# Optimization experiments

Hardware: AMD Instinct MI355X
Metric: run time of the kernel (lower is better)

## Reference

```python
import jax, jax.numpy as jnp
import numpy as np

D_MODEL = 256
N_LAYERS = 4
D_STATE = 16
EXPAND = 2
D_CONV = 4
D_INNER = EXPAND * D_MODEL
DT_RANK = (D_MODEL + 15) // 16  # ceil(d_model/16) = 16
BATCH = 8
SEQ = 2048
EPS = 1e-5


def setup_inputs() -> dict:
    key = jax.random.key(0)
    ks = jax.random.split(key, 12)
    rn = lambda k, s, sc=0.02: jax.random.normal(k, s, dtype=jnp.float32) * sc
    A_log = jnp.log(jnp.broadcast_to(jnp.arange(1, D_STATE + 1, dtype=jnp.float32),
                                     (N_LAYERS, D_INNER, D_STATE)))
    return {
        "x": jax.random.normal(ks[0], (BATCH, SEQ, 2), dtype=jnp.float32),
        "w_in": rn(ks[1], (D_MODEL, 2), 0.5),
        "b_in": jnp.zeros((D_MODEL,), jnp.float32),
        "norm_w": jnp.ones((N_LAYERS, D_MODEL), jnp.float32),
        "in_proj_w": rn(ks[2], (N_LAYERS, 2 * D_INNER, D_MODEL)),
        "conv_w": rn(ks[3], (N_LAYERS, D_INNER, 1, D_CONV), 0.1),
        "conv_b": jnp.zeros((N_LAYERS, D_INNER), jnp.float32),
        "x_proj_w": rn(ks[4], (N_LAYERS, DT_RANK + 2 * D_STATE, D_INNER)),
        "dt_proj_w": rn(ks[5], (N_LAYERS, D_INNER, DT_RANK), 0.1),
        "dt_proj_b": rn(ks[6], (N_LAYERS, D_INNER), 0.1),
        "A_log": A_log,
        "D_skip": jnp.ones((N_LAYERS, D_INNER), jnp.float32),
        "out_proj_w": rn(ks[7], (N_LAYERS, D_MODEL, D_INNER)),
        "w_head": rn(ks[8], (1, D_MODEL), 0.1),
        "b_head": jnp.zeros((1,), jnp.float32),
    }


def _rmsnorm(x, w):
    return x * jax.lax.rsqrt(jnp.mean(x * x, axis=-1, keepdims=True) + EPS) * w


def _causal_dw_conv(x, w, b):
    # x: (B, L, C); w: (C, 1, K) depthwise; causal left-pad K-1
    xt = jnp.swapaxes(x, 1, 2)  # (B, C, L)
    y = jax.lax.conv_general_dilated(xt, w, (1,), [(D_CONV - 1, 0)],
                                     dimension_numbers=("NCH", "OIH", "NCH"),
                                     feature_group_count=D_INNER)
    return jnp.swapaxes(y + b[None, :, None], 1, 2)


def _selective_scan(u, delta, A, Bm, Cm, Dp):
    # u, delta: (B, L, E); A: (E, N); Bm, Cm: (B, L, N); Dp: (E,)
    dA = jnp.exp(delta[..., None] * A)                 # (B, L, E, N)
    dBu = (delta * u)[..., None] * Bm[:, :, None, :]   # (B, L, E, N)

    def step(h, t):
        dA_t, dBu_t = t
        h = dA_t * h + dBu_t
        return h, h

    h0 = jnp.zeros((u.shape[0], A.shape[0], A.shape[1]), u.dtype)
    _, hs = jax.lax.scan(step, h0, (jnp.swapaxes(dA, 0, 1), jnp.swapaxes(dBu, 0, 1)))
    y = jnp.einsum("lben,bln->ble", hs, Cm)            # (B, L, E)
    return y + u * Dp


def _mamba_block(x, in_w, cw, cb, xp_w, dtw, dtb, A_log, Dp, out_w):
    xz = x @ in_w.T                                    # (B, L, 2E)
    u, z = jnp.split(xz, 2, axis=-1)
    u = jax.nn.silu(_causal_dw_conv(u, cw, cb))
    dbc = u @ xp_w.T                                   # (B, L, dt_rank + 2N)
    delta = jax.nn.softplus(dbc[..., :DT_RANK] @ dtw.T + dtb)
    Bm = dbc[..., DT_RANK:DT_RANK + D_STATE]
    Cm = dbc[..., DT_RANK + D_STATE:]
    y = _selective_scan(u, delta, -jnp.exp(A_log), Bm, Cm, Dp)
    return (y * jax.nn.silu(z)) @ out_w.T


def reference(x, w_in, b_in, norm_w, in_proj_w, conv_w, conv_b, x_proj_w,
              dt_proj_w, dt_proj_b, A_log, D_skip, out_proj_w, w_head, b_head):
    h = x @ w_in.T + b_in                              # (B, L, d_model)
    for i in range(N_LAYERS):
        h = h + _mamba_block(_rmsnorm(h, norm_w[i]), in_proj_w[i], conv_w[i],
                             conv_b[i], x_proj_w[i], dt_proj_w[i], dt_proj_b[i],
                             A_log[i], D_skip[i], out_proj_w[i])
    return (h @ w_head.T + b_head)[..., 0]             # (B, L)
```

## Files before the change

kernel.cpp:

```cpp
#include <hip/hip_runtime.h>
#include <hip/hip_bf16.h>

#define BATCH 8
#define SEQ   2048
#define DM    256
#define DI    512
#define DS    16
#define DTR   16
#define NL    4
#define ROWS  (BATCH*SEQ)
#define NCH   32
#define CHL   64
#define NF    576

typedef __attribute__((ext_vector_type(8))) __bf16 bh8;
typedef __attribute__((ext_vector_type(4))) float f4;

#if __has_builtin(__builtin_amdgcn_exp2f)
#define EXP2(x) __builtin_amdgcn_exp2f(x)
#else
#define EXP2(x) exp2f(x)
#endif
#define LOG2E 1.4426950408889634f

__device__ __forceinline__ float bf2f(unsigned short u) {
    union { unsigned int i; float f; } v; v.i = ((unsigned int)u) << 16; return v.f;
}
__device__ __forceinline__ float4 us4f(ushort4 q) {
    return make_float4(bf2f(q.x), bf2f(q.y), bf2f(q.z), bf2f(q.w));
}
__device__ __forceinline__ float ldg1(const void* p, int i, int bf) {
    if (bf) return bf2f(((const unsigned short*)p)[i]);
    return ((const float*)p)[i];
}
__device__ __forceinline__ float4 ldg4(const void* p, int i, int bf) {
    if (bf) return us4f(*(const ushort4*)(((const unsigned short*)p) + i));
    return *(const float4*)(((const float*)p) + i);
}
__device__ __forceinline__ unsigned short f2bs(float f) {
    union { float f; unsigned u; } x; x.f = f;
    unsigned r = (x.u + 0x7fffu + ((x.u >> 16) & 1u)) >> 16;
    return (unsigned short)r;
}
__device__ __forceinline__ float fsilu(float x) {
    return x * __builtin_amdgcn_rcpf(1.0f + __expf(-x));
}
__device__ __forceinline__ float fsoftplus(float x) {
    return (x > 15.0f) ? x : __logf(1.0f + __expf(x));
}
__device__ __forceinline__ void pow16(float e1, float* pw) {
    float p2 = e1 * e1, p3 = p2 * e1, p4 = p2 * p2;
    float p5 = p4 * e1, p6 = p4 * p2, p7 = p4 * p3, p8 = p4 * p4;
    pw[0] = e1; pw[1] = p2; pw[2] = p3; pw[3] = p4;
    pw[4] = p5; pw[5] = p6; pw[6] = p7; pw[7] = p8;
    pw[8]  = p8 * e1; pw[9]  = p8 * p2; pw[10] = p8 * p3; pw[11] = p8 * p4;
    pw[12] = p8 * p5; pw[13] = p8 * p6; pw[14] = p8 * p7; pw[15] = p8 * p8;
}

typedef const __attribute__((address_space(1))) unsigned int* gas_t;
typedef __attribute__((address_space(3))) unsigned int* las_t;
__device__ __forceinline__ void gl16(const void* g, void* l) {
    __builtin_amdgcn_global_load_lds((gas_t)g, (las_t)l, 16, 0, 0);
}

__global__ void k_probe(const void* x, const void* A_log, int* flag) {
    int t = threadIdx.x;
    float v = bf2f(((const unsigned short*)x)[2 * t]);
    int bad = (fabsf(v) < 32.0f) ? 0 : 1;
    for (int o = 1; o < 64; o <<= 1) bad += __shfl_xor(bad, o);
    int bf = (bad > 8) ? 0 : 1;
    int nb = 0;
    for (int j = 0; j < 64; j++) {
        int e = ((j * 64 + t) * 17) & 32767;
        int n = e & 15;
        float a = ldg1(A_log, e, bf);
        float ea = __expf(a);
        if (fabsf(ea - (float)(n + 1)) > 0.02f * (float)(n + 1)) nb = 1;
    }
    for (int o = 1; o < 64; o <<= 1) nb += __shfl_xor(nb, o);
    if (t == 0) { flag[0] = bf; flag[1] = (nb == 0) ? 1 : 0; }
}

__global__ __launch_bounds__(256) void k_prep(const void* dtw, const void* xpw,
                                              unsigned short* Wc, const int* flag) {
    int bf = *flag;
    int blk = blockIdx.x;
    int l = blk / NF, r = blk % NF;
    int t = threadIdx.x;
    unsigned short* out = Wc + ((size_t)l * NF + r) * DI;
#pragma unroll
    for (int p = 0; p < 2; p++) {
        int k = t + p * 256;
        float v = 0.0f;
        if (r < 512) {
            const int db = l * DI * DTR + r * DTR;
            const int xb = l * 48 * DI;
#pragma unroll
            for (int j = 0; j < 16; j++)
                v = fmaf(ldg1(dtw, db + j, bf), ldg1(xpw, xb + j * DI + k, bf), v);
        } else if (r < 544) {
            v = ldg1(xpw, l * 48 * DI + (16 + r - 512) * DI + k, bf);
        }
        out[k] = f2bs(v);
    }
}

__global__ __launch_bounds__(256) void k_inproj(const void* x, const void* w_in,
                                                const void* b_in, unsigned short* h, const int* flag) {
    int bf = *flag;
    int row = blockIdx.x, e = threadIdx.x;
    float x0 = ldg1(x, row * 2 + 0, bf), x1 = ldg1(x, row * 2 + 1, bf);
    float w0 = ldg1(w_in, e * 2 + 0, bf), w1 = ldg1(w_in, e * 2 + 1, bf);
    float bb = ldg1(b_in, e, bf);
    h[(size_t)row * DM + e] = f2bs(fmaf(x0, w0, fmaf(x1, w1, bb)));
}

__global__ __launch_bounds__(256) void k_rmsnorm(const unsigned short* h, const void* norm_w,
                                                 int w_off, unsigned short* xn, const int* flag) {
    int bf = *flag;
    int wv = threadIdx.x >> 6, ln = threadIdx.x & 63;
    int row = blockIdx.x * 4 + wv;
    float4 v = us4f(*(const ushort4*)(h + (size_t)row * DM + ln * 4));
    float ss = v.x * v.x + v.y * v.y + v.z * v.z + v.w * v.w;
    for (int o = 1; o < 64; o <<= 1) ss += __shfl_xor(ss, o);
    float sc = rsqrtf(ss / DM + 1e-5f);
    float4 w = ldg4(norm_w, w_off + ln * 4, bf);
    ushort4 o4 = { f2bs(v.x * sc * w.x), f2bs(v.y * sc * w.y),
                   f2bs(v.z * sc * w.z), f2bs(v.w * sc * w.w) };
    *(ushort4*)(xn + (size_t)row * DM + ln * 4) = o4;
}

#define ASTR 72

template <int BN, bool ADD>
__global__ __launch_bounds__(256, 4) void k_mfma(const unsigned short* A, const void* W, int w_off,
                                                 unsigned short* Cp, int N, int K, const int* flag) {
    int bf = *flag;
    __shared__ unsigned short SMEM[(128 + BN) * ASTR];
    unsigned short* As = SMEM;
    unsigned short* Ws = SMEM + 128 * 64;
    constexpr int NT = BN / 32;
    constexpr int TSTR = BN + 8;

    int bm = blockIdx.x, bn = blockIdx.y;
    int t = threadIdx.x;
    int w = t >> 6, lane = t & 63;
    int wm = w >> 1, wn = w & 1;
    int lr = lane & 15, quad = lane >> 4;
    int crow = lane >> 3;
    int ccol = ((lane & 7) ^ (lane >> 3)) * 8;

    f4 acc[4][NT];
#pragma unroll
    for (int i = 0; i < 4; i++)
#pragma unroll
        for (int j = 0; j < NT; j++) acc[i][j] = f4{0.f, 0.f, 0.f, 0.f};

    for (int k0 = 0; k0 < K; k0 += 64) {
        __syncthreads();
#pragma unroll
        for (int i = 0; i < 4; i++) {
            int ci = w * 4 + i;
            int r = ci * 8 + crow;
            gl16(A + (size_t)(bm * 128 + r) * K + k0 + ccol, &As[ci * 512]);
        }
        if (bf) {
#pragma unroll
            for (int i = 0; i < BN / 32; i++) {
                int ci = w * (BN / 32) + i;
                int r = ci * 8 + crow;
                gl16((const unsigned short*)W + (size_t)w_off +
                         (size_t)(bn * BN + r) * K + k0 + ccol,
                     &Ws[ci * 512]);
            }
        } else {
#pragma unroll
            for (int i = 0; i < BN * 8 / 256; i++) {
                int ch = t + i * 256;
                int r = ch >> 3, kc = (ch & 7) * 8;
                size_t off = (size_t)w_off + (size_t)(bn * BN + r) * K + k0 + kc;
                const float* src = (const float*)W + off;
                float4 a0 = *(const float4*)src;
                float4 a1 = *(const float4*)(src + 4);
                ushort4 v0 = { f2bs(a0.x), f2bs(a0.y), f2bs(a0.z), f2bs(a0.w) };
                ushort4 v1 = { f2bs(a1.x), f2bs(a1.y), f2bs(a1.z), f2bs(a1.w) };
                unsigned short* dst = &Ws[r * 64 + (kc ^ ((r & 7) << 3))];
                *(ushort4*)dst = v0;
                *(ushort4*)(dst + 4) = v1;
            }
        }
        __syncthreads();
#pragma unroll
        for (int ks = 0; ks < 64; ks += 32) {
            int csw = (ks + quad * 8) ^ ((lr & 7) << 3);
            bh8 af[4];
#pragma unroll
            for (int i = 0; i < 4; i++)
                af[i] = *(const bh8*)&As[(wm * 64 + i * 16 + lr) * 64 + csw];
            bh8 wf[NT];
#pragma unroll
            for (int j = 0; j < NT; j++)
                wf[j] = *(const bh8*)&Ws[(wn * (BN / 2) + j * 16 + lr) * 64 + csw];
#pragma unroll
            for (int i = 0; i < 4; i++)
#pragma unroll
                for (int j = 0; j < NT; j++)
                    acc[i][j] = __builtin_amdgcn_mfma_f32_16x16x32_bf16(af[i], wf[j], acc[i][j], 0, 0, 0);
        }
    }
    __syncthreads();
    unsigned short* Tile = SMEM;
#pragma unroll
    for (int i = 0; i < 4; i++) {
        int rl = wm * 64 + i * 16 + quad * 4;
#pragma unroll
        for (int j = 0; j < NT; j++) {
            int cl = wn * (BN / 2) + j * 16 + lr;
#pragma unroll
            for (int r = 0; r < 4; r++)
                Tile[(rl + r) * TSTR + cl] = f2bs(acc[i][j][r]);
        }
    }
    __syncthreads();
    constexpr int CPT = 128 * BN / 8 / 256;
#pragma unroll
    for (int i = 0; i < CPT; i++) {
        int ch = t + i * 256;
        int r = ch / (BN / 8), qc = (ch % (BN / 8)) * 8;
        uint4 v = *(uint4*)&Tile[r * TSTR + qc];
        size_t gidx = (size_t)(bm * 128 + r) * N + bn * BN + qc;
        if (ADD) {
            uint4 c = *(uint4*)&Cp[gidx];
            unsigned short* vp = (unsigned short*)&v;
            unsigned short* cp2 = (unsigned short*)&c;
            uint4 o;
            unsigned short* op = (unsigned short*)&o;
#pragma unroll
            for (int e = 0; e < 8; e++) op[e] = f2bs(bf2f(vp[e]) + bf2f(cp2[e]));
            *(uint4*)&Cp[gidx] = o;
        } else {
            *(uint4*)&Cp[gidx] = v;
        }
    }
}

__global__ __launch_bounds__(256, 4) void k_fused(const unsigned short* A, const unsigned short* Wc,
                                                  int w_off, unsigned short* delta, float* BC,
                                                  const void* dtb, int layer, const int* flag) {
    int bf = *flag;
    __shared__ unsigned short SMEM[(128 + 64) * ASTR];
    unsigned short* As = SMEM;
    unsigned short* Ws = SMEM + 128 * 64;
    constexpr int TSTR = 72;

    int bm = blockIdx.x, bn = blockIdx.y;
    int t = threadIdx.x;
    int w = t >> 6, lane = t & 63;
    int wm = w >> 1, wn = w & 1;
    int lr = lane & 15, quad = lane >> 4;
    int crow = lane >> 3;
    int ccol = ((lane & 7) ^ (lane >> 3)) * 8;

    f4 acc[4][2];
#pragma unroll
    for (int i = 0; i < 4; i++)
#pragma unroll
        for (int j = 0; j < 2; j++) acc[i][j] = f4{0.f, 0.f, 0.f, 0.f};

    for (int k0 = 0; k0 < DI; k0 += 64) {
        __syncthreads();
#pragma unroll
        for (int i = 0; i < 4; i++) {
            int ci = w * 4 + i;
            int r = ci * 8 + crow;
            gl16(A + (size_t)(bm * 128 + r) * DI + k0 + ccol, &As[ci * 512]);
        }
#pragma unroll
        for (int i = 0; i < 2; i++) {
            int ci = w * 2 + i;
            int r = ci * 8 + crow;
            gl16(Wc + (size_t)w_off + (size_t)(bn * 64 + r) * DI + k0 + ccol, &Ws[ci * 512]);
        }
        __syncthreads();
#pragma unroll
        for (int ks = 0; ks < 64; ks += 32) {
            int csw = (ks + quad * 8) ^ ((lr & 7) << 3);
            bh8 af[4];
#pragma unroll
            for (int i = 0; i < 4; i++)
                af[i] = *(const bh8*)&As[(wm * 64 + i * 16 + lr) * 64 + csw];
            bh8 wf[2];
#pragma unroll
            for (int j = 0; j < 2; j++)
                wf[j] = *(const bh8*)&Ws[(wn * 32 + j * 16 + lr) * 64 + csw];
#pragma unroll
            for (int i = 0; i < 4; i++)
#pragma unroll
                for (int j = 0; j < 2; j++)
                    acc[i][j] = __builtin_amdgcn_mfma_f32_16x16x32_bf16(af[i], wf[j], acc[i][j], 0, 0, 0);
        }
    }
    if (bn < 8) {
        __syncthreads();
        unsigned short* Tile = SMEM;
#pragma unroll
        for (int i = 0; i < 4; i++) {
            int rl = wm * 64 + i * 16 + quad * 4;
#pragma unroll
            for (int j = 0; j < 2; j++) {
                int cl = wn * 32 + j * 16 + lr;
                float bb = ldg1(dtb, layer * DI + bn * 64 + cl, bf);
#pragma unroll
                for (int r = 0; r < 4; r++)
                    Tile[(rl + r) * TSTR + cl] = f2bs(fsoftplus(acc[i][j][r] + bb));
            }
        }
        __syncthreads();
#pragma unroll
        for (int i = 0; i < 4; i++) {
            int ch = t + i * 256;
            int r = ch >> 3, qc = (ch & 7) * 8;
            uint4 v = *(uint4*)&Tile[r * TSTR + qc];
            *(uint4*)&delta[(size_t)(bm * 128 + r) * DI + bn * 64 + qc] = v;
        }
    } else {
#pragma unroll
        for (int i = 0; i < 4; i++) {
            int row0 = bm * 128 + wm * 64 + i * 16 + quad * 4;
#pragma unroll
            for (int j = 0; j < 2; j++) {
                int col = bn * 64 + wn * 32 + j * 16 + lr;
                if (col < 544) {
#pragma unroll
                    for (int r = 0; r < 4; r++)
                        BC[(size_t)(row0 + r) * 32 + (col - 512)] = acc[i][j][r];
                }
            }
        }
    }
}

__global__ __launch_bounds__(256) void k_conv(const unsigned short* xz, const void* cw, const void* cb,
                                              int layer, unsigned short* u, const int* flag) {
    int bf = *flag;
    int idx = blockIdx.x * 256 + threadIdx.x;
    int dq = idx & 127;
    int row = idx >> 7;
    int l = row & (SEQ - 1);
    int d = dq * 4;
    float4 w0 = ldg4(cw, (layer * DI + d + 0) * 4, bf);
    float4 w1 = ldg4(cw, (layer * DI + d + 1) * 4, bf);
    float4 w2 = ldg4(cw, (layer * DI + d + 2) * 4, bf);
    float4 w3 = ldg4(cw, (layer * DI + d + 3) * 4, bf);
    float4 bb = ldg4(cb, layer * DI + d, bf);
    const unsigned short* base = xz + (size_t)row * (2 * DI) + d;
    float4 t0 = make_float4(0, 0, 0, 0), t1 = t0, t2 = t0;
    if (l >= 3) t0 = us4f(*(const ushort4*)(base - 3 * 2 * DI));
    if (l >= 2) t1 = us4f(*(const ushort4*)(base - 2 * 2 * DI));
    if (l >= 1) t2 = us4f(*(const ushort4*)(base - 1 * 2 * DI));
    float4 t3 = us4f(*(const ushort4*)base);
    float a0 = bb.x; a0 = fmaf(w0.x, t0.x, a0); a0 = fmaf(w0.y, t1.x, a0); a0 = fmaf(w0.z, t2.x, a0); a0 = fmaf(w0.w, t3.x, a0);
    float a1 = bb.y; a1 = fmaf(w1.x, t0.y, a1); a1 = fmaf(w1.y, t1.y, a1); a1 = fmaf(w1.z, t2.y, a1); a1 = fmaf(w1.w, t3.y, a1);
    float a2 = bb.z; a2 = fmaf(w2.x, t0.z, a2); a2 = fmaf(w2.y, t1.z, a2); a2 = fmaf(w2.z, t2.z, a2); a2 = fmaf(w2.w, t3.z, a2);
    float a3 = bb.w; a3 = fmaf(w3.x, t0.w, a3); a3 = fmaf(w3.y, t1.w, a3); a3 = fmaf(w3.z, t2.w, a3); a3 = fmaf(w3.w, t3.w, a3);
    ushort4 o = { f2bs(fsilu(a0)), f2bs(fsilu(a1)), f2bs(fsilu(a2)), f2bs(fsilu(a3)) };
    *(ushort4*)(u + (size_t)row * DI + d) = o;
}

__global__ __launch_bounds__(256) void k_scan1(const unsigned short* delta, const unsigned short* u,
                                               const float* BC, const void* A_log, float* Sb, float* E,
                                               int layer, const int* flag) {
    int bf = flag[0], sA = flag[1];
    int x = blockIdx.x;
    int dg = x & 1, c = (x >> 1) & (NCH - 1), b = x >> 6;
    int tid = threadIdx.x;
    int d = dg * 256 + tid;
    int t0 = c * CHL;

    __shared__ float sB[CHL][16];
    {
        int r = tid >> 2, q = tid & 3;
        *(float4*)&sB[r][q * 4] =
            *(const float4*)(BC + ((size_t)b * SEQ + t0 + r) * 32 + q * 4);
    }

    float A2[16];
#pragma unroll
    for (int n4 = 0; n4 < 4; n4++) {
        float4 a4 = ldg4(A_log, (layer * DI + d) * DS + n4 * 4, bf);
        A2[n4 * 4 + 0] = -__expf(a4.x) * LOG2E;
        A2[n4 * 4 + 1] = -__expf(a4.y) * LOG2E;
        A2[n4 * 4 + 2] = -__expf(a4.z) * LOG2E;
        A2[n4 * 4 + 3] = -__expf(a4.w) * LOG2E;
    }
    float h[16];
#pragma unroll
    for (int n = 0; n < 16; n++) h[n] = 0.0f;
    float S = 0.0f;

    const unsigned short* dp = delta + ((size_t)b * SEQ + t0) * DI + d;
    const unsigned short* up = u + ((size_t)b * SEQ + t0) * DI + d;

    float dl0[4], uu0[4];
#pragma unroll
    for (int j = 0; j < 4; j++) { dl0[j] = bf2f(dp[j * DI]); uu0[j] = bf2f(up[j * DI]); }
    __syncthreads();

    for (int s = 0; s < CHL / 4; s++) {
        int sn = (s + 1 < CHL / 4) ? (s + 1) : s;
        float dl1[4], uu1[4];
#pragma unroll
        for (int j = 0; j < 4; j++) {
            dl1[j] = bf2f(dp[(sn * 4 + j) * DI]);
            uu1[j] = bf2f(up[(sn * 4 + j) * DI]);
        }
#pragma unroll
        for (int j = 0; j < 4; j++) {
            int t = s * 4 + j;
            float dlt = dl0[j], uu = uu0[j];
            float du = dlt * uu;
            S += dlt;
            if (sA) {
                float pw[16];
                pow16(EXP2(-dlt * LOG2E), pw);
#pragma unroll
                for (int n4 = 0; n4 < 4; n4++) {
                    float4 Bv = *(const float4*)&sB[t][n4 * 4];
                    int n = n4 * 4;
                    h[n + 0] = fmaf(pw[n + 0], h[n + 0], du * Bv.x);
                    h[n + 1] = fmaf(pw[n + 1], h[n + 1], du * Bv.y);
                    h[n + 2] = fmaf(pw[n + 2], h[n + 2], du * Bv.z);
                    h[n + 3] = fmaf(pw[n + 3], h[n + 3], du * Bv.w);
                }
            } else {
#pragma unroll
                for (int n4 = 0; n4 < 4; n4++) {
                    float4 Bv = *(const float4*)&sB[t][n4 * 4];
                    int n = n4 * 4;
                    float a0 = EXP2(dlt * A2[n + 0]); h[n + 0] = fmaf(a0, h[n + 0], du * Bv.x);
                    float a1 = EXP2(dlt * A2[n + 1]); h[n + 1] = fmaf(a1, h[n + 1], du * Bv.y);
                    float a2 = EXP2(dlt * A2[n + 2]); h[n + 2] = fmaf(a2, h[n + 2], du * Bv.z);
                    float a3 = EXP2(dlt * A2[n + 3]); h[n + 3] = fmaf(a3, h[n + 3], du * Bv.w);
                }
            }
        }
#pragma unroll
        for (int j = 0; j < 4; j++) { dl0[j] = dl1[j]; uu0[j] = uu1[j]; }
    }
    Sb[((size_t)b * NCH + c) * DI + d] = S;
    float* Ed = E + (((size_t)b * NCH + c) * DI + d) * DS;
#pragma unroll
    for (int n4 = 0; n4 < 4; n4++)
        *(float4*)(Ed + n4 * 4) = make_float4(h[n4 * 4], h[n4 * 4 + 1], h[n4 * 4 + 2], h[n4 * 4 + 3]);
}

__global__ __launch_bounds__(256) void k_stitch(const float* Sb, const void* A_log, float* E,
                                                int layer, const int* flag) {
    int bf = flag[0];
    int g = blockIdx.x * 256 + threadIdx.x;
    int b = g >> 13, r = g & 8191;
    int d = r >> 4;
    float A2a = -__expf(ldg1(A_log, (layer * DI + d) * DS + (r & 15), bf)) * LOG2E;
    size_t ebase = (size_t)b * NCH * (DI * DS) + r;
    float H = 0.0f;
    for (int c = 0; c < NCH; c++) {
        float p = EXP2(A2a * Sb[((size_t)b * NCH + c) * DI + d]);
        size_t idx = ebase + (size_t)c * (DI * DS);
        float e = E[idx];
        E[idx] = H;
        H = fmaf(p, H, e);
    }
}

__global__ __launch_bounds__(256) void k_scan2(const unsigned short* delta, const unsigned short* u,
                                               const float* BC, const void* A_log, const void* D_skip,
                                               const unsigned short* xz, const float* E,
                                               unsigned short* g, int layer, const int* flag) {
    int bf = flag[0], sA = flag[1];
    int x = blockIdx.x;
    int dg = x & 1, c = (x >> 1) & (NCH - 1), b = x >> 6;
    int tid = threadIdx.x;
    int d = dg * 256 + tid;
    int t0 = c * CHL;

    __shared__ float sBC[CHL][32];
#pragma unroll
    for (int k2 = 0; k2 < 2; k2++) {
        int fi = k2 * 256 + tid;
        int r = fi >> 3, q = fi & 7;
        *(float4*)&sBC[r][q * 4] =
            *(const float4*)(BC + ((size_t)b * SEQ + t0 + r) * 32 + q * 4);
    }

    float A2[16];
#pragma unroll
    for (int n4 = 0; n4 < 4; n4++) {
        float4 a4 = ldg4(A_log, (layer * DI + d) * DS + n4 * 4, bf);
        A2[n4 * 4 + 0] = -__expf(a4.x) * LOG2E;
        A2[n4 * 4 + 1] = -__expf(a4.y) * LOG2E;
        A2[n4 * 4 + 2] = -__expf(a4.z) * LOG2E;
        A2[n4 * 4 + 3] = -__expf(a4.w) * LOG2E;
    }
    float Dp = ldg1(D_skip, layer * DI + d, bf);

    float h[16];
    const float* E0 = E + (((size_t)b * NCH + c) * DI + d) * DS;
#pragma unroll
    for (int n4 = 0; n4 < 4; n4++) {
        float4 h4 = *(const float4*)(E0 + n4 * 4);
        h[n4 * 4 + 0] = h4.x; h[n4 * 4 + 1] = h4.y; h[n4 * 4 + 2] = h4.z; h[n4 * 4 + 3] = h4.w;
    }

    const unsigned short* dp = delta + ((size_t)b * SEQ + t0) * DI + d;
    const unsigned short* up = u + ((size_t)b * SEQ + t0) * DI + d;
    const unsigned short* zp = xz + ((size_t)b * SEQ + t0) * (2 * DI) + DI + d;
    unsigned short* gp = g + ((size_t)b * SEQ + t0) * DI + d;

    float dl0[4], uu0[4], zz0[4];
#pragma unroll
    for (int j = 0; j < 4; j++) {
        dl0[j] = bf2f(dp[j * DI]); uu0[j] = bf2f(up[j * DI]); zz0[j] = bf2f(zp[j * (2 * DI)]);
    }
    __syncthreads();

    for (int s = 0; s < CHL / 4; s++) {
        int sn = (s + 1 < CHL / 4) ? (s + 1) : s;
        float dl1[4], uu1[4], zz1[4];
#pragma unroll
        for (int j = 0; j < 4; j++) {
            dl1[j] = bf2f(dp[(sn * 4 + j) * DI]);
            uu1[j] = bf2f(up[(sn * 4 + j) * DI]);
            zz1[j] = bf2f(zp[(sn * 4 + j) * (2 * DI)]);
        }
#pragma unroll
        for (int j = 0; j < 4; j++) {
            int t = s * 4 + j;
            float dlt = dl0[j], uu = uu0[j], zz = zz0[j];
            float du = dlt * uu;
            float y = 0.0f;
            if (sA) {
                float pw[16];
                pow16(EXP2(-dlt * LOG2E), pw);
#pragma unroll
                for (int n4 = 0; n4 < 4; n4++) {
                    float4 Bv = *(const float4*)&sBC[t][n4 * 4];
                    float4 Cv = *(const float4*)&sBC[t][16 + n4 * 4];
                    int n = n4 * 4;
                    h[n + 0] = fmaf(pw[n + 0], h[n + 0], du * Bv.x); y = fmaf(Cv.x, h[n + 0], y);
                    h[n + 1] = fmaf(pw[n + 1], h[n + 1], du * Bv.y); y = fmaf(Cv.y, h[n + 1], y);
                    h[n + 2] = fmaf(pw[n + 2], h[n + 2], du * Bv.z); y = fmaf(Cv.z, h[n + 2], y);
                    h[n + 3] = fmaf(pw[n + 3], h[n + 3], du * Bv.w); y = fmaf(Cv.w, h[n + 3], y);
                }
            } else {
#pragma unroll
                for (int n4 = 0; n4 < 4; n4++) {
                    float4 Bv = *(const float4*)&sBC[t][n4 * 4];
                    float4 Cv = *(const float4*)&sBC[t][16 + n4 * 4];
                    int n = n4 * 4;
                    float a0 = EXP2(dlt * A2[n + 0]); h[n + 0] = fmaf(a0, h[n + 0], du * Bv.x); y = fmaf(Cv.x, h[n + 0], y);
                    float a1 = EXP2(dlt * A2[n + 1]); h[n + 1] = fmaf(a1, h[n + 1], du * Bv.y); y = fmaf(Cv.y, h[n + 1], y);
                    float a2 = EXP2(dlt * A2[n + 2]); h[n + 2] = fmaf(a2, h[n + 2], du * Bv.z); y = fmaf(Cv.z, h[n + 2], y);
                    float a3 = EXP2(dlt * A2[n + 3]); h[n + 3] = fmaf(a3, h[n + 3], du * Bv.w); y = fmaf(Cv.w, h[n + 3], y);
                }
            }
            float yt = fmaf(uu, Dp, y);
            gp[(size_t)t * DI] = f2bs(yt * fsilu(zz));
        }
#pragma unroll
        for (int j = 0; j < 4; j++) { dl0[j] = dl1[j]; uu0[j] = uu1[j]; zz0[j] = zz1[j]; }
    }
}

__global__ __launch_bounds__(256) void k_head(const unsigned short* h, const void* w_head,
                                              const void* b_head, void* out, const int* flag) {
    int bf = *flag;
    int wv = threadIdx.x >> 6, ln = threadIdx.x & 63;
    int row = blockIdx.x * 4 + wv;
    float4 v = us4f(*(const ushort4*)(h + (size_t)row * DM + ln * 4));
    float4 w = ldg4(w_head, ln * 4, bf);
    float s = v.x * w.x + v.y * w.y + v.z * w.z + v.w * w.w;
    for (int o = 1; o < 64; o <<= 1) s += __shfl_xor(s, o);
    if (ln == 0) {
        s += ldg1(b_head, 0, bf);
        if (bf) ((__hip_bfloat16*)out)[row] = __float2bfloat16(s);
        else    ((float*)out)[row] = s;
    }
}

extern "C" void kernel_launch(void* const* d_in, const int* in_sizes, int n_in,
                              void* d_out, int out_size, void* d_ws, size_t ws_size,
                              hipStream_t stream) {
    (void)in_sizes; (void)n_in; (void)out_size; (void)ws_size;
    const void* x      = d_in[0];
    const void* w_in   = d_in[1];
    const void* b_in   = d_in[2];
    const void* norm_w = d_in[3];
    const void* ipw    = d_in[4];
    const void* cw     = d_in[5];
    const void* cb     = d_in[6];
    const void* xpw    = d_in[7];
    const void* dtw    = d_in[8];
    const void* dtb    = d_in[9];
    const void* A_log  = d_in[10];
    const void* D_skip = d_in[11];
    const void* opw    = d_in[12];
    const void* w_head = d_in[13];
    const void* b_head = d_in[14];

    float* ws    = (float*)d_ws;
    unsigned short* h     = (unsigned short*)ws;
    unsigned short* xn    = (unsigned short*)(ws + 4194304);
    float*          Sb    = ws + 4194304;
    float*          E     = ws + 4718592;
    unsigned short* xz    = (unsigned short*)(ws + 8388608);
    unsigned short* u     = (unsigned short*)(ws + 25165824);
    float*          BC    = ws + 33554432;
    unsigned short* delta = (unsigned short*)(ws + 34340864);
    unsigned short* Wcomb = (unsigned short*)(ws + 38535168);
    int*            flag  = (int*)(ws + 42729472);

    k_probe<<<1, 64, 0, stream>>>(x, A_log, flag);
    k_prep<<<NL * NF, 256, 0, stream>>>(dtw, xpw, Wcomb, flag);
    k_inproj<<<ROWS, 256, 0, stream>>>(x, w_in, b_in, h, flag);

    for (int layer = 0; layer < NL; layer++) {
        k_rmsnorm<<<ROWS / 4, 256, 0, stream>>>(h, norm_w, layer * DM, xn, flag);
        k_mfma<128, false><<<dim3(ROWS / 128, 2 * DI / 128), 256, 0, stream>>>(
            xn, ipw, layer * 2 * DI * DM, xz, 2 * DI, DM, flag);
        k_conv<<<ROWS * DI / 4 / 256, 256, 0, stream>>>(xz, cw, cb, layer, u, flag);
        k_fused<<<dim3(ROWS / 128, NF / 64), 256, 0, stream>>>(
            u, Wcomb, layer * NF * DI, delta, BC, dtb, layer, flag);
        k_scan1<<<BATCH * NCH * 2, 256, 0, stream>>>(delta, u, BC, A_log, Sb, E, layer, flag);
        k_stitch<<<BATCH * DI * DS / 256, 256, 0, stream>>>(Sb, A_log, E, layer, flag);
        k_scan2<<<BATCH * NCH * 2, 256, 0, stream>>>(delta, u, BC, A_log, D_skip, xz, E,
                                                     u , layer, flag);
        k_mfma<64, true><<<dim3(ROWS / 128, DM / 64), 256, 0, stream>>>(
            u, opw, layer * DM * DI, h, DM, DI, flag);
    }

    k_head<<<ROWS / 4, 256, 0, stream>>>(h, w_head, b_head, d_out, flag);
}
```

Measured before the change: 643.1 us.

## Fold RMSNorm into in-proj GEMM via precomputed row sum-of-squares

Removes the standalone RMSNorm kernel that ran once per layer. The norm weight is folded into a bf16 copy of the in-proj weights, built once up front. Per-row partial sums of squares are produced in the epilogues of the input projection and the out-proj residual add, and the in-proj GEMM applies the rsqrt scale to its accumulators before writing. This saves a full read and write of the normalized activations and one launch per layer. In exchange it adds a weight-prep kernel, extra epilogue shuffles, and a reuse of the Sb workspace region for the row sums.

```diff
diff --git a/kernel.cpp b/kernel.cpp
--- a/kernel.cpp
+++ b/kernel.cpp
@@ -105,36 +105,38 @@
     }
 }
 
-__global__ __launch_bounds__(256) void k_inproj(const void* x, const void* w_in,
-                                                const void* b_in, unsigned short* h, const int* flag) {
+__global__ __launch_bounds__(256) void k_prepw(const void* ipw, const void* norm_w,
+                                               unsigned short* Wip, const int* flag) {
+    int bf = *flag;
+    int blk = blockIdx.x;
+    int l = blk >> 10, r = blk & 1023;
+    int t = threadIdx.x;
+    float v = ldg1(ipw, (l * 1024 + r) * 256 + t, bf) * ldg1(norm_w, l * 256 + t, bf);
+    Wip[((size_t)l * 1024 + r) * 256 + t] = f2bs(v);
+}
+
+__global__ __launch_bounds__(256) void k_inproj(const void* x, const void* w_in, const void* b_in,
+                                                unsigned short* h, float* rssq, const int* flag) {
     int bf = *flag;
     int row = blockIdx.x, e = threadIdx.x;
     float x0 = ldg1(x, row * 2 + 0, bf), x1 = ldg1(x, row * 2 + 1, bf);
     float w0 = ldg1(w_in, e * 2 + 0, bf), w1 = ldg1(w_in, e * 2 + 1, bf);
     float bb = ldg1(b_in, e, bf);
-    h[(size_t)row * DM + e] = f2bs(fmaf(x0, w0, fmaf(x1, w1, bb)));
-}
-
-__global__ __launch_bounds__(256) void k_rmsnorm(const unsigned short* h, const void* norm_w,
-                                                 int w_off, unsigned short* xn, const int* flag) {
-    int bf = *flag;
-    int wv = threadIdx.x >> 6, ln = threadIdx.x & 63;
-    int row = blockIdx.x * 4 + wv;
-    float4 v = us4f(*(const ushort4*)(h + (size_t)row * DM + ln * 4));
-    float ss = v.x * v.x + v.y * v.y + v.z * v.z + v.w * v.w;
+    unsigned short hb = f2bs(fmaf(x0, w0, fmaf(x1, w1, bb)));
+    h[(size_t)row * DM + e] = hb;
+    float hv = bf2f(hb);
+    float ss = hv * hv;
+#pragma unroll
     for (int o = 1; o < 64; o <<= 1) ss += __shfl_xor(ss, o);
-    float sc = rsqrtf(ss / DM + 1e-5f);
-    float4 w = ldg4(norm_w, w_off + ln * 4, bf);
-    ushort4 o4 = { f2bs(v.x * sc * w.x), f2bs(v.y * sc * w.y),
-                   f2bs(v.z * sc * w.z), f2bs(v.w * sc * w.w) };
-    *(ushort4*)(xn + (size_t)row * DM + ln * 4) = o4;
+    if ((e & 63) == 0) rssq[(size_t)row * 4 + (e >> 6)] = ss;
 }
 
 #define ASTR 72
 
-template <int BN, bool ADD>
+template <int BN, bool ADD, bool SCALE, bool RSUM, bool WINT>
 __global__ __launch_bounds__(256, 4) void k_mfma(const unsigned short* A, const void* W, int w_off,
-                                                 unsigned short* Cp, int N, int K, const int* flag) {
+                                                 unsigned short* Cp, float* rssq,
+                                                 int N, int K, const int* flag) {
     int bf = *flag;
     __shared__ unsigned short SMEM[(128 + BN) * ASTR];
     unsigned short* As = SMEM;
@@ -164,7 +166,7 @@
             int r = ci * 8 + crow;
             gl16(A + (size_t)(bm * 128 + r) * K + k0 + ccol, &As[ci * 512]);
         }
-        if (bf) {
+        if (WINT || bf) {
 #pragma unroll
             for (int i = 0; i < BN / 32; i++) {
                 int ci = w * (BN / 32) + i;
@@ -213,12 +215,23 @@
 #pragma unroll
     for (int i = 0; i < 4; i++) {
         int rl = wm * 64 + i * 16 + quad * 4;
+        float sc4[4];
+        if (SCALE) {
+#pragma unroll
+            for (int r = 0; r < 4; r++) {
+                float4 q4 = *(const float4*)&rssq[(size_t)(bm * 128 + rl + r) * 4];
+                sc4[r] = rsqrtf((q4.x + q4.y + q4.z + q4.w) * (1.0f / (float)DM) + 1e-5f);
+            }
+        }
 #pragma unroll
         for (int j = 0; j < NT; j++) {
             int cl = wn * (BN / 2) + j * 16 + lr;
 #pragma unroll
-            for (int r = 0; r < 4; r++)
-                Tile[(rl + r) * TSTR + cl] = f2bs(acc[i][j][r]);
+            for (int r = 0; r < 4; r++) {
+                float vv = acc[i][j][r];
+                if (SCALE) vv *= sc4[r];
+                Tile[(rl + r) * TSTR + cl] = f2bs(vv);
+            }
         }
     }
     __syncthreads();
@@ -233,11 +246,20 @@
             uint4 c = *(uint4*)&Cp[gidx];
             unsigned short* vp = (unsigned short*)&v;
             unsigned short* cp2 = (unsigned short*)&c;
-            uint4 o;
-            unsigned short* op = (unsigned short*)&o;
-#pragma unroll
-            for (int e = 0; e < 8; e++) op[e] = f2bs(bf2f(vp[e]) + bf2f(cp2[e]));
-            *(uint4*)&Cp[gidx] = o;
+            uint4 ov;
+            unsigned short* op = (unsigned short*)&ov;
+            float ssq = 0.0f;
+#pragma unroll
+            for (int e = 0; e < 8; e++) {
+                op[e] = f2bs(bf2f(vp[e]) + bf2f(cp2[e]));
+                if (RSUM) { float hv = bf2f(op[e]); ssq = fmaf(hv, hv, ssq); }
+            }
+            *(uint4*)&Cp[gidx] = ov;
+            if (RSUM) {
+#pragma unroll
+                for (int o2 = 1; o2 < 8; o2 <<= 1) ssq += __shfl_xor(ssq, o2);
+                if ((lane & 7) == 0) rssq[(size_t)(bm * 128 + r) * 4 + bn] = ssq;
+            }
         } else {
             *(uint4*)&Cp[gidx] = v;
         }
@@ -609,7 +631,7 @@
 
     float* ws    = (float*)d_ws;
     unsigned short* h     = (unsigned short*)ws;
-    unsigned short* xn    = (unsigned short*)(ws + 4194304);
+    float*          rssq  = ws + 4194304;
     float*          Sb    = ws + 4194304;
     float*          E     = ws + 4718592;
     unsigned short* xz    = (unsigned short*)(ws + 8388608);
@@ -617,16 +639,17 @@
     float*          BC    = ws + 33554432;
     unsigned short* delta = (unsigned short*)(ws + 34340864);
     unsigned short* Wcomb = (unsigned short*)(ws + 38535168);
+    unsigned short* Wipc  = (unsigned short*)(ws + 39124992);
     int*            flag  = (int*)(ws + 42729472);
 
     k_probe<<<1, 64, 0, stream>>>(x, A_log, flag);
     k_prep<<<NL * NF, 256, 0, stream>>>(dtw, xpw, Wcomb, flag);
-    k_inproj<<<ROWS, 256, 0, stream>>>(x, w_in, b_in, h, flag);
+    k_prepw<<<NL * 1024, 256, 0, stream>>>(ipw, norm_w, Wipc, flag);
+    k_inproj<<<ROWS, 256, 0, stream>>>(x, w_in, b_in, h, rssq, flag);
 
     for (int layer = 0; layer < NL; layer++) {
-        k_rmsnorm<<<ROWS / 4, 256, 0, stream>>>(h, norm_w, layer * DM, xn, flag);
-        k_mfma<128, false><<<dim3(ROWS / 128, 2 * DI / 128), 256, 0, stream>>>(
-            xn, ipw, layer * 2 * DI * DM, xz, 2 * DI, DM, flag);
+        k_mfma<128, false, true, false, true><<<dim3(ROWS / 128, 2 * DI / 128), 256, 0, stream>>>(
+            h, Wipc, layer * 2 * DI * DM, xz, rssq, 2 * DI, DM, flag);
         k_conv<<<ROWS * DI / 4 / 256, 256, 0, stream>>>(xz, cw, cb, layer, u, flag);
         k_fused<<<dim3(ROWS / 128, NF / 64), 256, 0, stream>>>(
             u, Wcomb, layer * NF * DI, delta, BC, dtb, layer, flag);
@@ -634,8 +657,8 @@
         k_stitch<<<BATCH * DI * DS / 256, 256, 0, stream>>>(Sb, A_log, E, layer, flag);
         k_scan2<<<BATCH * NCH * 2, 256, 0, stream>>>(delta, u, BC, A_log, D_skip, xz, E,
                                                      u , layer, flag);
-        k_mfma<64, true><<<dim3(ROWS / 128, DM / 64), 256, 0, stream>>>(
-            u, opw, layer * DM * DI, h, DM, DI, flag);
+        k_mfma<64, true, false, true, false><<<dim3(ROWS / 128, DM / 64), 256, 0, stream>>>(
+            u, opw, layer * DM * DI, h, rssq, DM, DI, flag);
     }
 
     k_head<<<ROWS / 4, 256, 0, stream>>>(h, w_head, b_head, d_out, flag);
```

New measurement: 587.7 us. 8.6% less time.
